# Optimization experiments

Hardware: AMD Instinct MI355X
Metric: run time of the kernel (lower is better)

Reference implementation:

```python
import jax, jax.numpy as jnp
import numpy as np

GAMMA = 1.0
BIG = 1e10  # finite stand-in for +inf so exp/log stay NaN-free under autodiff


def _pairwise_sq_dist(X, Y):
    # X: (na, T, d), Y: (nb, T, d) -> D: (na, nb, T, T) squared euclidean
    sqx = jnp.sum(X * X, axis=-1)                      # (na, T)
    sqy = jnp.sum(Y * Y, axis=-1)                      # (nb, T)
    cross = jnp.einsum('atd,bsd->abts', X, Y)          # (na, nb, T, T)
    return sqx[:, None, :, None] + sqy[None, :, None, :] - 2.0 * cross


def _soft_dtw(D, gamma):
    # D: (B, T, T) -> (B,) soft-DTW values, anti-diagonal wavefront via lax.scan.
    B, T, _ = D.shape
    inv_g = 1.0 / gamma
    idx = jnp.arange(T)

    def step(carry, p):
        prev2, prev1 = carry                           # diagonals p-2, p-1: (B, T)
        j = p - idx
        valid = (j >= 0) & (j < T)
        d = D[:, idx, jnp.clip(j, 0, T - 1)]           # (B, T) costs on diag p
        # shifted neighbors: prev2[i-1] (diag), prev1[i-1] (up), prev1[i] (left)
        corner = jnp.where(p == 0, 0.0, BIG)           # R[0,0] = 0 boundary
        prev2_s = jnp.concatenate([jnp.broadcast_to(corner, (B, 1)), prev2[:, :-1]], axis=1)
        prev1_s = jnp.concatenate([jnp.full((B, 1), BIG, D.dtype), prev1[:, :-1]], axis=1)
        r0 = -prev2_s * inv_g
        r1 = -prev1_s * inv_g
        r2 = -prev1 * inv_g
        rmax = jnp.maximum(jnp.maximum(r0, r1), r2)
        rsum = jnp.exp(r0 - rmax) + jnp.exp(r1 - rmax) + jnp.exp(r2 - rmax)
        softmin = -gamma * (jnp.log(rsum) + rmax)
        new = jnp.where(valid[None, :], d + softmin, BIG)
        return (prev1, new), None

    init = (jnp.full((B, T), BIG, D.dtype), jnp.full((B, T), BIG, D.dtype))
    (_, last), _ = jax.lax.scan(step, init, jnp.arange(2 * T - 1))
    return last[:, T - 1]                              # R[T, T]


def setup_inputs() -> dict:
    key = jax.random.key(0)
    kx, ky = jax.random.split(key)
    X = jax.random.normal(kx, (128, 128, 8), dtype=jnp.float32)
    Y = jax.random.normal(ky, (16, 128, 8), dtype=jnp.float32)
    return {"X": X, "Y": Y}


def reference(X, Y):
    na, T, _ = X.shape
    nb = Y.shape[0]
    D = _pairwise_sq_dist(X, Y).reshape(na * nb, T, T)
    dist = _soft_dtw(D, GAMMA)
    return dist.reshape(na, nb)
```

## Files before the change

### kernel.cpp

```cpp
#include <hip/hip_runtime.h>

#define T 128
#define L2E 1.4426950408889634f
#define LN2F 0.6931471805599453f

typedef _Float16 h2 __attribute__((ext_vector_type(2)));

__device__ __forceinline__ float shr1(float x) {
    return __int_as_float(__builtin_amdgcn_update_dpp(
        0, __float_as_int(x), 0x138, 0xF, 0xF, true));
}

template <int CTRL>
__device__ __forceinline__ float dppmax(float x) {
    float t = __int_as_float(__builtin_amdgcn_update_dpp(
        __float_as_int(x), __float_as_int(x), CTRL, 0xF, 0xF, false));
    return fmaxf(x, t);
}

struct RowR { float u, v, w, z, s; };

__device__ __forceinline__ float dot2(h2 x, float ybits, float acc) {
    return __builtin_amdgcn_fdot2(x, __builtin_bit_cast(h2, ybits), acc, false);
}

__launch_bounds__(256)
__global__ void sdtw_kernel(const float* __restrict__ X,
                            const float* __restrict__ Y,
                            float* __restrict__ out) {
    __shared__ float lds[4 * 1960];
    const int lane = threadIdx.x & 63;
    const int w    = threadIdx.x >> 6;
    const int pair = blockIdx.x * 4 + w;
    const int a = pair >> 4;
    const int b = pair & 15;

    float* E = lds + w * 1960;
    float* O = E + 980;

    {
        const float* ybase = Y + (size_t)b * T * 8;
        for (int r = lane; r < 386; r += 64) {
            float4 pk; pk.x = 0.f; pk.y = 0.f; pk.z = 0.f; pk.w = 0.f;
            float sq = -3.0e37f;
            int j = r - 126;
            if (j >= 0 && j < T) {
                const float4* src = (const float4*)(ybase + j * 8);
                float4 y0 = src[0], y1 = src[1];
                float s = y0.x*y0.x + y0.y*y0.y + y0.z*y0.z + y0.w*y0.w
                        + y1.x*y1.x + y1.y*y1.y + y1.z*y1.z + y1.w*y1.w;
                const float c = 2.0f * L2E;
                h2 a0 = { (_Float16)(c*y0.x), (_Float16)(c*y0.y) };
                h2 a1 = { (_Float16)(c*y0.z), (_Float16)(c*y0.w) };
                h2 a2 = { (_Float16)(c*y1.x), (_Float16)(c*y1.y) };
                h2 a3 = { (_Float16)(c*y1.z), (_Float16)(c*y1.w) };
                pk.x = __builtin_bit_cast(float, a0);
                pk.y = __builtin_bit_cast(float, a1);
                pk.z = __builtin_bit_cast(float, a2);
                pk.w = __builtin_bit_cast(float, a3);
                sq = -L2E * s;
            }
            float* reg = (r & 1) ? O : E;
            int h = r >> 1;
            reg[h]       = pk.x;
            reg[196 + h] = pk.y;
            reg[392 + h] = pk.z;
            reg[588 + h] = pk.w;
            reg[784 + h] = sq;
        }
    }

    h2 xe0, xe1, xe2, xe3, xo0, xo1, xo2, xo3;
    float lsxe, lsxo;
    {
        const float* xb = X + ((size_t)a * T + 2 * lane) * 8;
        const float4* s0p = (const float4*)xb;
        float4 v0 = s0p[0], v1 = s0p[1], u0 = s0p[2], u1 = s0p[3];
        xe0 = h2{ (_Float16)v0.x, (_Float16)v0.y };
        xe1 = h2{ (_Float16)v0.z, (_Float16)v0.w };
        xe2 = h2{ (_Float16)v1.x, (_Float16)v1.y };
        xe3 = h2{ (_Float16)v1.z, (_Float16)v1.w };
        lsxe = -L2E * (v0.x*v0.x+v0.y*v0.y+v0.z*v0.z+v0.w*v0.w
                      +v1.x*v1.x+v1.y*v1.y+v1.z*v1.z+v1.w*v1.w);
        xo0 = h2{ (_Float16)u0.x, (_Float16)u0.y };
        xo1 = h2{ (_Float16)u0.z, (_Float16)u0.w };
        xo2 = h2{ (_Float16)u1.x, (_Float16)u1.y };
        xo3 = h2{ (_Float16)u1.z, (_Float16)u1.w };
        lsxo = -L2E * (u0.x*u0.x+u0.y*u0.y+u0.z*u0.z+u0.w*u0.w
                      +u1.x*u1.x+u1.y*u1.y+u1.z*u1.z+u1.w*u1.w);
    }

    __syncthreads();

#define FETCH(SL, B, C) {            \
    SL.u = (B)[(C)];                 \
    SL.v = (B)[196 + (C)];           \
    SL.w = (B)[392 + (C)];           \
    SL.z = (B)[588 + (C)];           \
    SL.s = (B)[784 + (C)];           \
}

    RowR s0, s1, s2, s3, s4, s5, s6, s7;
    {
        int h0 = 63 - lane;
        FETCH(s0, E, h0);     FETCH(s1, O, h0);
        FETCH(s2, E, h0 + 1); FETCH(s3, O, h0 + 1);
        FETCH(s4, E, h0 + 2); FETCH(s5, O, h0 + 2);
        FETCH(s6, E, h0 + 3); FETCH(s7, O, h0 + 3);
    }
    const float* pe = E + (67 - lane);
    const float* po = O + (67 - lane);

    float fe0 = 0.f, fo0 = 0.f, fo1 = 0.f;
    int off = 90;
    float fe1;
    {
        float acc = lsxe + s0.s;
        acc = dot2(xe0, s0.u, acc);
        acc = dot2(xe1, s0.v, acc);
        acc = dot2(xe2, s0.w, acc);
        acc = dot2(xe3, s0.z, acc);
        fe1 = __builtin_amdgcn_exp2f(acc) * 0x1p90f;
    }

#define BODY(PE1, PE2, PO1, PO2, RO, RE) {              \
    float sB = shr1(PO1);                               \
    float sA = shr1(PO2);                               \
    float ae = lsxe + RE.s;                             \
    ae = dot2(xe0, RE.u, ae);                           \
    ae = dot2(xe1, RE.v, ae);                           \
    ae = dot2(xe2, RE.w, ae);                           \
    ae = dot2(xe3, RE.z, ae);                           \
    float ao = lsxo + RO.s;                             \
    ao = dot2(xo0, RO.u, ao);                           \
    ao = dot2(xo1, RO.v, ao);                           \
    ao = dot2(xo2, RO.w, ao);                           \
    ao = dot2(xo3, RO.z, ao);                           \
    float Ee = __builtin_amdgcn_exp2f(ae);              \
    float Eo = __builtin_amdgcn_exp2f(ao);              \
    float Se = Ee * ((sA + sB) + PE1);                  \
    float So = Eo * ((PE2 + PE1) + PO1);                \
    PE2 = Se; PO2 = So;                                 \
}

#define RENORM() {                                                            \
    float mx = fmaxf(fmaxf(fe0, fe1), fmaxf(fo0, fo1));                       \
    mx = dppmax<0x111>(mx);                                    \
    mx = dppmax<0x112>(mx);                                    \
    mx = dppmax<0x114>(mx);                                    \
    mx = dppmax<0x118>(mx);                                    \
    int r0_ = __builtin_amdgcn_readlane(__float_as_int(mx), 15);              \
    int r1_ = __builtin_amdgcn_readlane(__float_as_int(mx), 31);              \
    int r2_ = __builtin_amdgcn_readlane(__float_as_int(mx), 47);              \
    int r3_ = __builtin_amdgcn_readlane(__float_as_int(mx), 63);              \
    int mb = max(max(r0_, r1_), max(r2_, r3_));                               \
    int e = ((mb >> 23) & 0xff) - 217;                \
    fe0 = ldexpf(fe0, -e); fe1 = ldexpf(fe1, -e);                             \
    fo0 = ldexpf(fo0, -e); fo1 = ldexpf(fo1, -e);                             \
    off -= e;                                                                 \
}

    for (int it = 0; it < 31; ++it) {
        BODY(fe1, fe0, fo1, fo0, s0, s1); FETCH(s0, pe, 0);
        BODY(fe0, fe1, fo0, fo1, s1, s2); FETCH(s1, po, 0);
        BODY(fe1, fe0, fo1, fo0, s2, s3); FETCH(s2, pe, 1);
        BODY(fe0, fe1, fo0, fo1, s3, s4); FETCH(s3, po, 1);
        RENORM();
        BODY(fe1, fe0, fo1, fo0, s4, s5); FETCH(s4, pe, 2);
        BODY(fe0, fe1, fo0, fo1, s5, s6); FETCH(s5, po, 2);
        BODY(fe1, fe0, fo1, fo0, s6, s7); FETCH(s6, pe, 3);
        BODY(fe0, fe1, fo0, fo1, s7, s0); FETCH(s7, po, 3);
        RENORM();
        pe += 4; po += 4;
    }
    BODY(fe1, fe0, fo1, fo0, s0, s1); FETCH(s0, pe, 0);
    BODY(fe0, fe1, fo0, fo1, s1, s2); FETCH(s1, po, 0);
    BODY(fe1, fe0, fo1, fo0, s2, s3); FETCH(s2, pe, 1);
    BODY(fe0, fe1, fo0, fo1, s3, s4); FETCH(s3, po, 1);
    RENORM();
    BODY(fe1, fe0, fo1, fo0, s4, s5);
    BODY(fe0, fe1, fo0, fo1, s5, s6);

    if (lane == 63)
        out[pair] = ((float)off - __builtin_amdgcn_logf(fo1)) * LN2F;
}

extern "C" void kernel_launch(void* const* d_in, const int* in_sizes, int n_in,
                              void* d_out, int out_size, void* d_ws, size_t ws_size,
                              hipStream_t stream) {
    const float* X = (const float*)d_in[0];
    const float* Y = (const float*)d_in[1];
    float* out = (float*)d_out;
    sdtw_kernel<<<512, 256, 0, stream>>>(X, Y, out);
}
```

Baseline: 86.59 us.

## Replace fp16 dot2 with fp32 FMA, interleave LDS rows, reuse shifted neighbor

Switches the distance dot products from packed fp16 fdot2 to full fp32 FMAs split into two independent chains, and changes the LDS layout from planar arrays to an interleaved per-row record of 10 floats read with float2 loads. It also carries the previous shifted value (sPrev) across iterations instead of issuing a second DPP shift per step, and rescales it in the renormalization. This improves accuracy and drops one DPP per step, but doubles the FMA count and the LDS footprint and traffic per row.

```diff
diff --git a/kernel.cpp b/kernel.cpp
--- a/kernel.cpp
+++ b/kernel.cpp
@@ -3,8 +3,7 @@
 #define T 128
 #define L2E 1.4426950408889634f
 #define LN2F 0.6931471805599453f
-
-typedef _Float16 h2 __attribute__((ext_vector_type(2)));
+#define SENT -3.0e37f
 
 __device__ __forceinline__ float shr1(float x) {
     return __int_as_float(__builtin_amdgcn_update_dpp(
@@ -18,128 +17,128 @@
     return fmaxf(x, t);
 }
 
-struct RowR { float u, v, w, z, s; };
-
-__device__ __forceinline__ float dot2(h2 x, float ybits, float acc) {
-    return __builtin_amdgcn_fdot2(x, __builtin_bit_cast(h2, ybits), acc, false);
-}
+struct RowF { float2 a, b, c, d; float s; };
 
 __launch_bounds__(256)
 __global__ void sdtw_kernel(const float* __restrict__ X,
                             const float* __restrict__ Y,
                             float* __restrict__ out) {
-    __shared__ float lds[4 * 1960];
+    __shared__ float lds[4 * 3920];
     const int lane = threadIdx.x & 63;
     const int w    = threadIdx.x >> 6;
     const int pair = blockIdx.x * 4 + w;
     const int a = pair >> 4;
     const int b = pair & 15;
 
-    float* E = lds + w * 1960;
-    float* O = E + 980;
+    float* E = lds + w * 3920;
+    float* O = E + 1960;
 
     {
         const float* ybase = Y + (size_t)b * T * 8;
-        for (int r = lane; r < 386; r += 64) {
-            float4 pk; pk.x = 0.f; pk.y = 0.f; pk.z = 0.f; pk.w = 0.f;
-            float sq = -3.0e37f;
-            int j = r - 126;
+        for (int idx = lane; idx < 392; idx += 64) {
+            int P = idx & 1, h = idx >> 1;
+            int j = 2 * h + P - 126;
+            float2 pa, pb, pc, pd;
+            pa.x = 0.f; pa.y = 0.f; pb.x = 0.f; pb.y = 0.f;
+            pc.x = 0.f; pc.y = 0.f; pd.x = 0.f; pd.y = 0.f;
+            float sq = SENT;
             if (j >= 0 && j < T) {
                 const float4* src = (const float4*)(ybase + j * 8);
                 float4 y0 = src[0], y1 = src[1];
                 float s = y0.x*y0.x + y0.y*y0.y + y0.z*y0.z + y0.w*y0.w
                         + y1.x*y1.x + y1.y*y1.y + y1.z*y1.z + y1.w*y1.w;
                 const float c = 2.0f * L2E;
-                h2 a0 = { (_Float16)(c*y0.x), (_Float16)(c*y0.y) };
-                h2 a1 = { (_Float16)(c*y0.z), (_Float16)(c*y0.w) };
-                h2 a2 = { (_Float16)(c*y1.x), (_Float16)(c*y1.y) };
-                h2 a3 = { (_Float16)(c*y1.z), (_Float16)(c*y1.w) };
-                pk.x = __builtin_bit_cast(float, a0);
-                pk.y = __builtin_bit_cast(float, a1);
-                pk.z = __builtin_bit_cast(float, a2);
-                pk.w = __builtin_bit_cast(float, a3);
+                pa.x = c*y0.x; pa.y = c*y0.y; pb.x = c*y0.z; pb.y = c*y0.w;
+                pc.x = c*y1.x; pc.y = c*y1.y; pd.x = c*y1.z; pd.y = c*y1.w;
                 sq = -L2E * s;
             }
-            float* reg = (r & 1) ? O : E;
-            int h = r >> 1;
-            reg[h]       = pk.x;
-            reg[196 + h] = pk.y;
-            reg[392 + h] = pk.z;
-            reg[588 + h] = pk.w;
-            reg[784 + h] = sq;
+            float* reg = (P ? O : E) + h * 10;
+            *(float2*)(reg)     = pa;
+            *(float2*)(reg + 2) = pb;
+            *(float2*)(reg + 4) = pc;
+            *(float2*)(reg + 6) = pd;
+            reg[8] = sq;
         }
     }
 
-    h2 xe0, xe1, xe2, xe3, xo0, xo1, xo2, xo3;
-    float lsxe, lsxo;
+    float xe0,xe1,xe2,xe3,xe4,xe5,xe6,xe7, lsxe;
+    float xo0,xo1,xo2,xo3,xo4,xo5,xo6,xo7, lsxo;
     {
         const float* xb = X + ((size_t)a * T + 2 * lane) * 8;
         const float4* s0p = (const float4*)xb;
         float4 v0 = s0p[0], v1 = s0p[1], u0 = s0p[2], u1 = s0p[3];
-        xe0 = h2{ (_Float16)v0.x, (_Float16)v0.y };
-        xe1 = h2{ (_Float16)v0.z, (_Float16)v0.w };
-        xe2 = h2{ (_Float16)v1.x, (_Float16)v1.y };
-        xe3 = h2{ (_Float16)v1.z, (_Float16)v1.w };
+        xe0=v0.x; xe1=v0.y; xe2=v0.z; xe3=v0.w;
+        xe4=v1.x; xe5=v1.y; xe6=v1.z; xe7=v1.w;
         lsxe = -L2E * (v0.x*v0.x+v0.y*v0.y+v0.z*v0.z+v0.w*v0.w
                       +v1.x*v1.x+v1.y*v1.y+v1.z*v1.z+v1.w*v1.w);
-        xo0 = h2{ (_Float16)u0.x, (_Float16)u0.y };
-        xo1 = h2{ (_Float16)u0.z, (_Float16)u0.w };
-        xo2 = h2{ (_Float16)u1.x, (_Float16)u1.y };
-        xo3 = h2{ (_Float16)u1.z, (_Float16)u1.w };
+        xo0=u0.x; xo1=u0.y; xo2=u0.z; xo3=u0.w;
+        xo4=u1.x; xo5=u1.y; xo6=u1.z; xo7=u1.w;
         lsxo = -L2E * (u0.x*u0.x+u0.y*u0.y+u0.z*u0.z+u0.w*u0.w
                       +u1.x*u1.x+u1.y*u1.y+u1.z*u1.z+u1.w*u1.w);
     }
 
     __syncthreads();
 
-#define FETCH(SL, B, C) {            \
-    SL.u = (B)[(C)];                 \
-    SL.v = (B)[196 + (C)];           \
-    SL.w = (B)[392 + (C)];           \
-    SL.z = (B)[588 + (C)];           \
-    SL.s = (B)[784 + (C)];           \
+#define FETCH(SL, B, K) {                          \
+    const float* q_ = (B) + (K) * 10;              \
+    SL.a = *(const float2*)(q_);                   \
+    SL.b = *(const float2*)(q_ + 2);               \
+    SL.c = *(const float2*)(q_ + 4);               \
+    SL.d = *(const float2*)(q_ + 6);               \
+    SL.s = q_[8];                                  \
 }
 
-    RowR s0, s1, s2, s3, s4, s5, s6, s7;
+    RowF s0, s1, s2, s3, s4, s5, s6, s7;
+    const int hb0 = 63 - lane;
     {
-        int h0 = 63 - lane;
-        FETCH(s0, E, h0);     FETCH(s1, O, h0);
-        FETCH(s2, E, h0 + 1); FETCH(s3, O, h0 + 1);
-        FETCH(s4, E, h0 + 2); FETCH(s5, O, h0 + 2);
-        FETCH(s6, E, h0 + 3); FETCH(s7, O, h0 + 3);
+        const float* Eh = E + hb0 * 10;
+        const float* Oh = O + hb0 * 10;
+        FETCH(s0, Eh, 0); FETCH(s1, Oh, 0);
+        FETCH(s2, Eh, 1); FETCH(s3, Oh, 1);
+        FETCH(s4, Eh, 2); FETCH(s5, Oh, 2);
+        FETCH(s6, Eh, 3); FETCH(s7, Oh, 3);
     }
-    const float* pe = E + (67 - lane);
-    const float* po = O + (67 - lane);
+    const float* pe = E + (67 - lane) * 10;
+    const float* po = O + (67 - lane) * 10;
 
-    float fe0 = 0.f, fo0 = 0.f, fo1 = 0.f;
+    float fe0 = 0.f, fo0 = 0.f, fo1 = 0.f, fe1;
+    float sPrev = 0.f;
     int off = 90;
-    float fe1;
     {
-        float acc = lsxe + s0.s;
-        acc = dot2(xe0, s0.u, acc);
-        acc = dot2(xe1, s0.v, acc);
-        acc = dot2(xe2, s0.w, acc);
-        acc = dot2(xe3, s0.z, acc);
-        fe1 = __builtin_amdgcn_exp2f(acc) * 0x1p90f;
+        float t0 = fmaf(xe0, s0.a.x, lsxe);
+        t0 = fmaf(xe1, s0.a.y, t0);
+        t0 = fmaf(xe2, s0.b.x, t0);
+        t0 = fmaf(xe3, s0.b.y, t0);
+        float t1 = fmaf(xe4, s0.c.x, s0.s);
+        t1 = fmaf(xe5, s0.c.y, t1);
+        t1 = fmaf(xe6, s0.d.x, t1);
+        t1 = fmaf(xe7, s0.d.y, t1);
+        fe1 = __builtin_amdgcn_exp2f(t0 + t1) * 0x1p90f;
     }
 
 #define BODY(PE1, PE2, PO1, PO2, RO, RE) {              \
+    float ae0 = fmaf(xe0, RE.a.x, lsxe);                \
+    ae0 = fmaf(xe1, RE.a.y, ae0);                       \
+    ae0 = fmaf(xe2, RE.b.x, ae0);                       \
+    ae0 = fmaf(xe3, RE.b.y, ae0);                       \
+    float ae1 = fmaf(xe4, RE.c.x, RE.s);                \
+    ae1 = fmaf(xe5, RE.c.y, ae1);                       \
+    ae1 = fmaf(xe6, RE.d.x, ae1);                       \
+    ae1 = fmaf(xe7, RE.d.y, ae1);                       \
+    float Ee = __builtin_amdgcn_exp2f(ae0 + ae1);       \
+    float ao0 = fmaf(xo0, RO.a.x, lsxo);                \
+    ao0 = fmaf(xo1, RO.a.y, ao0);                       \
+    ao0 = fmaf(xo2, RO.b.x, ao0);                       \
+    ao0 = fmaf(xo3, RO.b.y, ao0);                       \
+    float ao1 = fmaf(xo4, RO.c.x, RO.s);                \
+    ao1 = fmaf(xo5, RO.c.y, ao1);                       \
+    ao1 = fmaf(xo6, RO.d.x, ao1);                       \
+    ao1 = fmaf(xo7, RO.d.y, ao1);                       \
+    float Eo = __builtin_amdgcn_exp2f(ao0 + ao1);       \
     float sB = shr1(PO1);                               \
-    float sA = shr1(PO2);                               \
-    float ae = lsxe + RE.s;                             \
-    ae = dot2(xe0, RE.u, ae);                           \
-    ae = dot2(xe1, RE.v, ae);                           \
-    ae = dot2(xe2, RE.w, ae);                           \
-    ae = dot2(xe3, RE.z, ae);                           \
-    float ao = lsxo + RO.s;                             \
-    ao = dot2(xo0, RO.u, ao);                           \
-    ao = dot2(xo1, RO.v, ao);                           \
-    ao = dot2(xo2, RO.w, ao);                           \
-    ao = dot2(xo3, RO.z, ao);                           \
-    float Ee = __builtin_amdgcn_exp2f(ae);              \
-    float Eo = __builtin_amdgcn_exp2f(ao);              \
-    float Se = Ee * ((sA + sB) + PE1);                  \
+    float Se = Ee * ((sPrev + sB) + PE1);               \
     float So = Eo * ((PE2 + PE1) + PO1);                \
+    sPrev = sB;                                         \
     PE2 = Se; PO2 = So;                                 \
 }
 
@@ -157,6 +156,7 @@
     int e = ((mb >> 23) & 0xff) - 217;                \
     fe0 = ldexpf(fe0, -e); fe1 = ldexpf(fe1, -e);                             \
     fo0 = ldexpf(fo0, -e); fo1 = ldexpf(fo1, -e);                             \
+    sPrev = ldexpf(sPrev, -e);         \
     off -= e;                                                                 \
 }
 
@@ -171,7 +171,7 @@
         BODY(fe1, fe0, fo1, fo0, s6, s7); FETCH(s6, pe, 3);
         BODY(fe0, fe1, fo0, fo1, s7, s0); FETCH(s7, po, 3);
         RENORM();
-        pe += 4; po += 4;
+        pe += 40; po += 40;
     }
     BODY(fe1, fe0, fo1, fo0, s0, s1); FETCH(s0, pe, 0);
     BODY(fe0, fe1, fo0, fo1, s1, s2); FETCH(s1, po, 0);
```

Result: slower. 95.64 us (+10.5%).
